# Optimization experiments

Measured on AMD Instinct MI355X. Metric: run time of the kernel, lower is better.

Reference implementation:

```python
import jax, jax.numpy as jnp
import numpy as np

B, C, W, H = 8, 256, 64, 64


def _conv1x1(x, w, b):
    # 1x1 conv == per-pixel channel GEMM. x: [B,C,W,H], w: [O,C], b: [O]
    return jnp.einsum('oc,bchw->bohw', w, x) + b[None, :, None, None]


def setup_inputs() -> dict:
    key = jax.random.key(0)
    ks = jax.random.split(key, 9)
    s = 1.0 / np.sqrt(C)
    return {
        'queries': jax.random.normal(ks[0], (B, C, W, H), dtype=jnp.float32),
        'keys': jax.random.normal(ks[1], (B, C, W, H), dtype=jnp.float32),
        'mask': jax.random.uniform(ks[2], (B, 1, W, H), dtype=jnp.float32),
        'Wq': jax.random.normal(ks[3], (C, C), dtype=jnp.float32) * s,
        'bq': jax.random.normal(ks[4], (C,), dtype=jnp.float32) * 0.01,
        'Wk': jax.random.normal(ks[5], (C, C), dtype=jnp.float32) * s,
        'bk': jax.random.normal(ks[6], (C,), dtype=jnp.float32) * 0.01,
        'Wv': jax.random.normal(ks[7], (C, C), dtype=jnp.float32) * s,
        'bv': jax.random.normal(ks[8], (C,), dtype=jnp.float32) * 0.01,
    }


def reference(queries, keys, mask, Wq, bq, Wk, bk, Wv, bv):
    b, c, w, h = queries.shape
    n = w * h
    q = _conv1x1(queries, Wq, bq).reshape(b, c, n)   # [B,C,N]
    k = _conv1x1(keys, Wk, bk).reshape(b, c, n)      # [B,C,N]
    v = _conv1x1(keys, Wv, bv).reshape(b, c, n)      # [B,C,N]
    # mask spatial size equals feature size -> interpolate(scale_factor=1) is identity
    m = mask.reshape(b, n)                            # [B,N]
    # scores[b,i,j] = <q_i, k_j>; torch's repeated mask multiplies row i by mask[i]
    scores = jnp.einsum('bcq,bck->bqk', q, k) * m[:, :, None]
    attn_w = jax.nn.softmax(scores, axis=-1)          # softmax over key dim
    attn = jnp.einsum('bqk,bck->bcq', attn_w, v).reshape(b, c, w, h)
    return queries * mask + (1.0 - mask) * attn
```

## Files before the change

kernel.cpp:

```cpp
#include <hip/hip_runtime.h>

typedef __attribute__((ext_vector_type(8))) _Float16 half8;
typedef __attribute__((ext_vector_type(4))) _Float16 half4;
typedef __attribute__((ext_vector_type(4))) float f32x4;

#define CDIM 256
#define NDIM 4096
#define MFMAH(a, b, c) __builtin_amdgcn_mfma_f32_16x16x32_f16((a), (b), (c), 0, 0, 0)

__global__ void cast_w_kernel(const float* __restrict__ Wq,
                              const float* __restrict__ Wk,
                              const float* __restrict__ Wv,
                              _Float16* __restrict__ Wc) {
  int t = blockIdx.x * 256 + threadIdx.x;
  int mat = t >> 14;
  int idx = (t & 16383) * 4;
  const float* W = (mat == 0) ? Wq : (mat == 1 ? Wk : Wv);
  float4 w = *(const float4*)(W + idx);
  half4 h = {(_Float16)w.x, (_Float16)w.y, (_Float16)w.z, (_Float16)w.w};
  *(half4*)(Wc + mat * 65536 + idx) = h;
}

__global__ __launch_bounds__(256, 2) void proj_kernel(
    const float* __restrict__ queries, const float* __restrict__ keys,
    const _Float16* __restrict__ Wc,
    const float* __restrict__ bq, const float* __restrict__ bk,
    const float* __restrict__ bv,
    _Float16* __restrict__ Qh, _Float16* __restrict__ Kh,
    _Float16* __restrict__ Vh)
{
  const int z = blockIdx.z, p = z >> 3, b = z & 7;
  const float* __restrict__ X = (p == 0) ? queries : keys;
  const _Float16* __restrict__ W = Wc + p * 65536;
  const float* __restrict__ bias = (p == 0) ? bq : (p == 1 ? bk : bv);
  const int n0 = blockIdx.x * 128;

  __shared__ __align__(16) _Float16 Xs[128][264];

  const int tid = threadIdx.x;
  const int wv = tid >> 6, lane = tid & 63, l16 = lane & 15, quad = lane >> 4;

#pragma unroll
  for (int it = 0; it < 32; ++it) {
    int id = tid + it * 256;
    int c = id >> 5, n4 = id & 31;
    float4 x = *(const float4*)&X[((size_t)(b * CDIM + c)) * NDIM + n0 + n4 * 4];
    Xs[n4 * 4 + 0][c] = (_Float16)x.x;
    Xs[n4 * 4 + 1][c] = (_Float16)x.y;
    Xs[n4 * 4 + 2][c] = (_Float16)x.z;
    Xs[n4 * 4 + 3][c] = (_Float16)x.w;
  }
  __syncthreads();

  f32x4 acc[4][8];
#pragma unroll
  for (int og = 0; og < 4; ++og)
#pragma unroll
    for (int ng = 0; ng < 8; ++ng) acc[og][ng] = (f32x4){0.f, 0.f, 0.f, 0.f};

#pragma unroll
  for (int kc = 0; kc < 8; ++kc) {
    half8 wf[4], xf[8];
#pragma unroll
    for (int og = 0; og < 4; ++og)
      wf[og] = *(const half8*)(W + (wv * 64 + og * 16 + l16) * CDIM + kc * 32 + quad * 8);
#pragma unroll
    for (int ng = 0; ng < 8; ++ng)
      xf[ng] = *(const half8*)&Xs[ng * 16 + l16][kc * 32 + quad * 8];
#pragma unroll
    for (int og = 0; og < 4; ++og)
#pragma unroll
      for (int ng = 0; ng < 8; ++ng)
        acc[og][ng] = MFMAH(wf[og], xf[ng], acc[og][ng]);
  }

#pragma unroll
  for (int og = 0; og < 4; ++og) {
    float4 b4 = *(const float4*)&bias[wv * 64 + og * 16 + quad * 4];
#pragma unroll
    for (int ng = 0; ng < 8; ++ng) {
      const int n = n0 + ng * 16 + l16;
      if (p == 2) {
#pragma unroll
        for (int r = 0; r < 4; ++r) {
          int o = wv * 64 + og * 16 + quad * 4 + r;
          float y = acc[og][ng][r] + ((const float*)&b4)[r];
          Vh[((size_t)(b * CDIM + o)) * NDIM + n] = (_Float16)y;
        }
      } else {
        half4 h4;
#pragma unroll
        for (int r = 0; r < 4; ++r)
          h4[r] = (_Float16)(acc[og][ng][r] + ((const float*)&b4)[r]);
        size_t idx = ((size_t)(b * NDIM + n)) * CDIM + wv * 64 + og * 16 + quad * 4;
        if (p == 0) *(half4*)&Qh[idx] = h4;
        else        *(half4*)&Kh[idx] = h4;
      }
    }
  }
}

__global__ __launch_bounds__(256, 2) void attn_kernel(
    const float* __restrict__ queries, const float* __restrict__ mask,
    const _Float16* __restrict__ Qh, const _Float16* __restrict__ Kh,
    const _Float16* __restrict__ Vh, float* __restrict__ out)
{
  const int blk = blockIdx.x, b = blk & 7, it = blk >> 3;
  const int i0 = it * 64;

  __shared__ __align__(16) _Float16 Ks[64][264];
  __shared__ __align__(16) _Float16 Vs[256][72];
  __shared__ __align__(16) _Float16 Ps[64][72];
  __shared__ __align__(16) float Al[64];
  __shared__ __align__(16) float Li[64];

  const int tid = threadIdx.x;
  const int wv = tid >> 6, lane = tid & 63, l16 = lane & 15, quad = lane >> 4;

  half8 qf[8];
  {
    const size_t qrow = ((size_t)(b * NDIM + i0 + wv * 16 + l16)) * CDIM;
#pragma unroll
    for (int kc = 0; kc < 8; ++kc)
      qf[kc] = *(const half8*)(Qh + qrow + kc * 32 + quad * 8);
  }
  const float mval = mask[(size_t)b * NDIM + i0 + wv * 16 + l16];
  float m_run = -1e30f, l_run = 0.f;

  f32x4 O[4][4];
#pragma unroll
  for (int g = 0; g < 4; ++g)
#pragma unroll
    for (int cg = 0; cg < 4; ++cg) O[g][cg] = (f32x4){0.f, 0.f, 0.f, 0.f};

  const _Float16* __restrict__ Kb = Kh + (size_t)b * NDIM * CDIM;
  const _Float16* __restrict__ Vbp = Vh + (size_t)b * CDIM * NDIM;

  for (int jt = 0; jt < 64; ++jt) {
    const int j0 = jt * 64;
    __syncthreads();
#pragma unroll
    for (int it2 = 0; it2 < 8; ++it2) {
      int id = tid + it2 * 256;
      int j = id >> 5, c8 = id & 31;
      *(uint4*)&Ks[j][c8 * 8] = *(const uint4*)(Kb + (size_t)(j0 + j) * CDIM + c8 * 8);
    }
#pragma unroll
    for (int it2 = 0; it2 < 8; ++it2) {
      int id = tid + it2 * 256;
      int c = id >> 3, j8 = id & 7;
      *(uint4*)&Vs[c][j8 * 8] = *(const uint4*)(Vbp + (size_t)c * NDIM + j0 + j8 * 8);
    }
    __syncthreads();

    f32x4 s[4];
#pragma unroll
    for (int js = 0; js < 4; ++js) s[js] = (f32x4){0.f, 0.f, 0.f, 0.f};
#pragma unroll
    for (int kc = 0; kc < 8; ++kc) {
#pragma unroll
      for (int js = 0; js < 4; ++js) {
        half8 kf = *(const half8*)&Ks[js * 16 + l16][kc * 32 + quad * 8];
        s[js] = MFMAH(kf, qf[kc], s[js]);
      }
    }

    float a[16];
    float mx = -1e30f;
#pragma unroll
    for (int js = 0; js < 4; ++js)
#pragma unroll
      for (int r = 0; r < 4; ++r) {
        float v = s[js][r] * mval;
        a[js * 4 + r] = v;
        mx = fmaxf(mx, v);
      }
    mx = fmaxf(mx, __shfl_xor(mx, 16));
    mx = fmaxf(mx, __shfl_xor(mx, 32));
    const float mnew = fmaxf(m_run, mx);
    const float alpha = __expf(m_run - mnew);
    m_run = mnew;
    float psum = 0.f;
#pragma unroll
    for (int js = 0; js < 4; ++js) {
      float p0 = __expf(a[js * 4 + 0] - mnew);
      float p1 = __expf(a[js * 4 + 1] - mnew);
      float p2 = __expf(a[js * 4 + 2] - mnew);
      float p3 = __expf(a[js * 4 + 3] - mnew);
      psum += (p0 + p1) + (p2 + p3);
      half4 hp = {(_Float16)p0, (_Float16)p1, (_Float16)p2, (_Float16)p3};
      *(half4*)&Ps[wv * 16 + l16][js * 16 + quad * 4] = hp;
    }
    psum += __shfl_xor(psum, 16);
    psum += __shfl_xor(psum, 32);
    l_run = l_run * alpha + psum;
    if (quad == 0) Al[wv * 16 + l16] = alpha;
    __syncthreads();

    f32x4 av[4];
#pragma unroll
    for (int g = 0; g < 4; ++g) av[g] = *(const f32x4*)&Al[g * 16 + quad * 4];
#pragma unroll
    for (int g = 0; g < 4; ++g)
#pragma unroll
      for (int cg = 0; cg < 4; ++cg)
#pragma unroll
        for (int r = 0; r < 4; ++r) O[g][cg][r] *= av[g][r];
#pragma unroll
    for (int kk = 0; kk < 2; ++kk) {
      half8 pa[4], vf[4];
#pragma unroll
      for (int g = 0; g < 4; ++g)
        pa[g] = *(const half8*)&Ps[g * 16 + l16][kk * 32 + quad * 8];
#pragma unroll
      for (int cg = 0; cg < 4; ++cg)
        vf[cg] = *(const half8*)&Vs[wv * 64 + cg * 16 + l16][kk * 32 + quad * 8];
#pragma unroll
      for (int g = 0; g < 4; ++g)
#pragma unroll
        for (int cg = 0; cg < 4; ++cg)
          O[g][cg] = MFMAH(pa[g], vf[cg], O[g][cg]);
    }
  }

  if (quad == 0) Li[wv * 16 + l16] = 1.0f / l_run;
  __syncthreads();
#pragma unroll
  for (int g = 0; g < 4; ++g) {
    f32x4 li4 = *(const f32x4*)&Li[g * 16 + quad * 4];
    const int i = i0 + g * 16 + quad * 4;
    float4 m4 = *(const float4*)&mask[(size_t)b * NDIM + i];
#pragma unroll
    for (int cg = 0; cg < 4; ++cg) {
      const int c = wv * 64 + cg * 16 + l16;
      const size_t base = ((size_t)(b * CDIM + c)) * NDIM + i;
      float4 q4 = *(const float4*)(queries + base);
      float4 o4;
      o4.x = q4.x * m4.x + (1.f - m4.x) * (O[g][cg][0] * li4[0]);
      o4.y = q4.y * m4.y + (1.f - m4.y) * (O[g][cg][1] * li4[1]);
      o4.z = q4.z * m4.z + (1.f - m4.z) * (O[g][cg][2] * li4[2]);
      o4.w = q4.w * m4.w + (1.f - m4.w) * (O[g][cg][3] * li4[3]);
      *(float4*)(out + base) = o4;
    }
  }
}

extern "C" void kernel_launch(void* const* d_in, const int* in_sizes, int n_in,
                              void* d_out, int out_size, void* d_ws, size_t ws_size,
                              hipStream_t stream) {
  const float* queries = (const float*)d_in[0];
  const float* keys    = (const float*)d_in[1];
  const float* mask    = (const float*)d_in[2];
  const float* Wq = (const float*)d_in[3];
  const float* bq = (const float*)d_in[4];
  const float* Wk = (const float*)d_in[5];
  const float* bk = (const float*)d_in[6];
  const float* Wv = (const float*)d_in[7];
  const float* bv = (const float*)d_in[8];
  float* out = (float*)d_out;

  const size_t elems = (size_t)8 * NDIM * CDIM;
  _Float16* Qh = (_Float16*)d_ws;
  _Float16* Kh = Qh + elems;
  _Float16* Vh = Kh + elems;
  _Float16* Wc = Vh + elems;

  cast_w_kernel<<<dim3(192), 256, 0, stream>>>(Wq, Wk, Wv, Wc);
  proj_kernel<<<dim3(32, 1, 24), 256, 0, stream>>>(
      queries, keys, Wc, bq, bk, bv, Qh, Kh, Vh);
  attn_kernel<<<dim3(512), 256, 0, stream>>>(
      queries, mask, Qh, Kh, Vh, out);
}
```

Measured before the change: 358.6 us.

## Use 32x32 MFMA for QK scores with split-key warps and restructure X loads

The QK^T score computation now uses 32x32x16 MFMA tiles. Each wave covers 32 query rows by 32 keys, so the key tile is split between wave pairs, and row max and sum are combined through shared memory at the cost of an extra barrier per tile. Separately, the projection kernel's X staging now reads one pixel column across 8 channels per thread and writes packed half8 values to LDS, replacing scattered scalar half stores. This trades fewer LDS operations per MFMA for more query registers (16 half8 fragments) and an additional synchronisation in the softmax step.

```diff
diff --git a/kernel.cpp b/kernel.cpp
--- a/kernel.cpp
+++ b/kernel.cpp
@@ -3,10 +3,12 @@
 typedef __attribute__((ext_vector_type(8))) _Float16 half8;
 typedef __attribute__((ext_vector_type(4))) _Float16 half4;
 typedef __attribute__((ext_vector_type(4))) float f32x4;
+typedef __attribute__((ext_vector_type(16))) float f32x16;
 
 #define CDIM 256
 #define NDIM 4096
 #define MFMAH(a, b, c) __builtin_amdgcn_mfma_f32_16x16x32_f16((a), (b), (c), 0, 0, 0)
+#define MFMA32(a, b, c) __builtin_amdgcn_mfma_f32_32x32x16_f16((a), (b), (c), 0, 0, 0)
 
 __global__ void cast_w_kernel(const float* __restrict__ Wq,
                               const float* __restrict__ Wk,
@@ -40,15 +42,17 @@
   const int tid = threadIdx.x;
   const int wv = tid >> 6, lane = tid & 63, l16 = lane & 15, quad = lane >> 4;
 
-#pragma unroll
-  for (int it = 0; it < 32; ++it) {
-    int id = tid + it * 256;
-    int c = id >> 5, n4 = id & 31;
-    float4 x = *(const float4*)&X[((size_t)(b * CDIM + c)) * NDIM + n0 + n4 * 4];
-    Xs[n4 * 4 + 0][c] = (_Float16)x.x;
-    Xs[n4 * 4 + 1][c] = (_Float16)x.y;
-    Xs[n4 * 4 + 2][c] = (_Float16)x.z;
-    Xs[n4 * 4 + 3][c] = (_Float16)x.w;
+  {
+    const int nn = tid & 127, ch = tid >> 7;
+#pragma unroll
+    for (int it2 = 0; it2 < 16; ++it2) {
+      const int c0 = it2 * 16 + ch * 8;
+      const float* src = X + ((size_t)(b * CDIM + c0)) * NDIM + n0 + nn;
+      half8 hx;
+#pragma unroll
+      for (int k = 0; k < 8; ++k) hx[k] = (_Float16)src[(size_t)k * NDIM];
+      *(half8*)&Xs[nn][c0] = hx;
+    }
   }
   __syncthreads();
 
@@ -113,18 +117,23 @@
   __shared__ __align__(16) _Float16 Ps[64][72];
   __shared__ __align__(16) float Al[64];
   __shared__ __align__(16) float Li[64];
+  __shared__ __align__(16) float Mp[2][64];
+  __shared__ __align__(16) float Sp[2][64];
 
   const int tid = threadIdx.x;
   const int wv = tid >> 6, lane = tid & 63, l16 = lane & 15, quad = lane >> 4;
-
-  half8 qf[8];
+  const int l32 = lane & 31, h = lane >> 5;
+  const int jq = wv & 1, iq = wv >> 1;
+  const int myi = iq * 32 + l32;
+
+  half8 qf[16];
   {
-    const size_t qrow = ((size_t)(b * NDIM + i0 + wv * 16 + l16)) * CDIM;
-#pragma unroll
-    for (int kc = 0; kc < 8; ++kc)
-      qf[kc] = *(const half8*)(Qh + qrow + kc * 32 + quad * 8);
-  }
-  const float mval = mask[(size_t)b * NDIM + i0 + wv * 16 + l16];
+    const size_t qrow = ((size_t)(b * NDIM + i0 + myi)) * CDIM;
+#pragma unroll
+    for (int kk = 0; kk < 16; ++kk)
+      qf[kk] = *(const half8*)(Qh + qrow + kk * 16 + h * 8);
+  }
+  const float mval = mask[(size_t)b * NDIM + i0 + myi];
   float m_run = -1e30f, l_run = 0.f;
 
   f32x4 O[4][4];
@@ -153,49 +162,42 @@
     }
     __syncthreads();
 
-    f32x4 s[4];
-#pragma unroll
-    for (int js = 0; js < 4; ++js) s[js] = (f32x4){0.f, 0.f, 0.f, 0.f};
-#pragma unroll
-    for (int kc = 0; kc < 8; ++kc) {
-#pragma unroll
-      for (int js = 0; js < 4; ++js) {
-        half8 kf = *(const half8*)&Ks[js * 16 + l16][kc * 32 + quad * 8];
-        s[js] = MFMAH(kf, qf[kc], s[js]);
-      }
-    }
-
-    float a[16];
+    f32x16 st = {};
+#pragma unroll
+    for (int kk = 0; kk < 16; ++kk) {
+      half8 kf = *(const half8*)&Ks[jq * 32 + l32][kk * 16 + h * 8];
+      st = MFMA32(kf, qf[kk], st);
+    }
+
     float mx = -1e30f;
 #pragma unroll
-    for (int js = 0; js < 4; ++js)
-#pragma unroll
-      for (int r = 0; r < 4; ++r) {
-        float v = s[js][r] * mval;
-        a[js * 4 + r] = v;
-        mx = fmaxf(mx, v);
-      }
-    mx = fmaxf(mx, __shfl_xor(mx, 16));
+    for (int r = 0; r < 16; ++r) mx = fmaxf(mx, st[r] * mval);
     mx = fmaxf(mx, __shfl_xor(mx, 32));
-    const float mnew = fmaxf(m_run, mx);
+    if (h == 0) Mp[jq][myi] = mx;
+    __syncthreads();
+
+    const float mxall = fmaxf(Mp[0][myi], Mp[1][myi]);
+    const float mnew = fmaxf(m_run, mxall);
     const float alpha = __expf(m_run - mnew);
     m_run = mnew;
+    if (jq == 0 && h == 0) Al[myi] = alpha;
+
     float psum = 0.f;
 #pragma unroll
-    for (int js = 0; js < 4; ++js) {
-      float p0 = __expf(a[js * 4 + 0] - mnew);
-      float p1 = __expf(a[js * 4 + 1] - mnew);
-      float p2 = __expf(a[js * 4 + 2] - mnew);
-      float p3 = __expf(a[js * 4 + 3] - mnew);
+    for (int g2 = 0; g2 < 4; ++g2) {
+      float p0 = __expf(st[g2 * 4 + 0] * mval - mnew);
+      float p1 = __expf(st[g2 * 4 + 1] * mval - mnew);
+      float p2 = __expf(st[g2 * 4 + 2] * mval - mnew);
+      float p3 = __expf(st[g2 * 4 + 3] * mval - mnew);
       psum += (p0 + p1) + (p2 + p3);
       half4 hp = {(_Float16)p0, (_Float16)p1, (_Float16)p2, (_Float16)p3};
-      *(half4*)&Ps[wv * 16 + l16][js * 16 + quad * 4] = hp;
-    }
-    psum += __shfl_xor(psum, 16);
+      *(half4*)&Ps[myi][jq * 32 + g2 * 8 + h * 4] = hp;
+    }
     psum += __shfl_xor(psum, 32);
-    l_run = l_run * alpha + psum;
-    if (quad == 0) Al[wv * 16 + l16] = alpha;
-    __syncthreads();
+    if (h == 0) Sp[jq][myi] = psum;
+    __syncthreads();
+
+    l_run = l_run * alpha + Sp[0][myi] + Sp[1][myi];
 
     f32x4 av[4];
 #pragma unroll
@@ -223,7 +225,7 @@
     }
   }
 
-  if (quad == 0) Li[wv * 16 + l16] = 1.0f / l_run;
+  if (jq == 0 && h == 0) Li[myi] = 1.0f / l_run;
   __syncthreads();
 #pragma unroll
   for (int g = 0; g < 4; ++g) {
```

Measured after the change: 535.8 us. +49.4%, slower.

## Load V fragments straight to registers and double-buffer P to drop a barrier

Applied to the files above, without the earlier changes.

Each wave now loads its own 64-channel slice of V from global memory directly into MFMA register fragments, instead of staging the whole V tile through shared memory. The P and alpha shared buffers are double-buffered by iteration parity, which removes the barrier at the top of the key-tile loop. This cuts LDS traffic and one block-wide sync per tile. In exchange, the V global loads are less coalesced (64-byte row segments), and 32 extra VGPRs stay live across the score MFMAs, which may cause spills under the two-blocks-per-CU launch bound.

```diff
diff --git a/kernel.cpp b/kernel.cpp
--- a/kernel.cpp
+++ b/kernel.cpp
@@ -109,9 +109,8 @@
   const int i0 = it * 64;
 
   __shared__ __align__(16) _Float16 Ks[64][264];
-  __shared__ __align__(16) _Float16 Vs[256][72];
-  __shared__ __align__(16) _Float16 Ps[64][72];
-  __shared__ __align__(16) float Al[64];
+  __shared__ __align__(16) _Float16 Ps[2][64][72];
+  __shared__ __align__(16) float Al[2][64];
   __shared__ __align__(16) float Li[64];
 
   const int tid = threadIdx.x;
@@ -134,23 +133,23 @@
     for (int cg = 0; cg < 4; ++cg) O[g][cg] = (f32x4){0.f, 0.f, 0.f, 0.f};
 
   const _Float16* __restrict__ Kb = Kh + (size_t)b * NDIM * CDIM;
-  const _Float16* __restrict__ Vbp = Vh + (size_t)b * CDIM * NDIM;
+  const _Float16* __restrict__ Vw = Vh + ((size_t)(b * CDIM + wv * 64)) * NDIM;
 
   for (int jt = 0; jt < 64; ++jt) {
     const int j0 = jt * 64;
-    __syncthreads();
+    const int pb = jt & 1;
 #pragma unroll
     for (int it2 = 0; it2 < 8; ++it2) {
       int id = tid + it2 * 256;
       int j = id >> 5, c8 = id & 31;
       *(uint4*)&Ks[j][c8 * 8] = *(const uint4*)(Kb + (size_t)(j0 + j) * CDIM + c8 * 8);
     }
-#pragma unroll
-    for (int it2 = 0; it2 < 8; ++it2) {
-      int id = tid + it2 * 256;
-      int c = id >> 3, j8 = id & 7;
-      *(uint4*)&Vs[c][j8 * 8] = *(const uint4*)(Vbp + (size_t)c * NDIM + j0 + j8 * 8);
-    }
+    half8 vf[2][4];
+#pragma unroll
+    for (int kk = 0; kk < 2; ++kk)
+#pragma unroll
+      for (int cg = 0; cg < 4; ++cg)
+        vf[kk][cg] = *(const half8*)(Vw + (size_t)(cg * 16 + l16) * NDIM + j0 + kk * 32 + quad * 8);
     __syncthreads();
 
     f32x4 s[4];
@@ -189,17 +188,17 @@
       float p3 = __expf(a[js * 4 + 3] - mnew);
       psum += (p0 + p1) + (p2 + p3);
       half4 hp = {(_Float16)p0, (_Float16)p1, (_Float16)p2, (_Float16)p3};
-      *(half4*)&Ps[wv * 16 + l16][js * 16 + quad * 4] = hp;
+      *(half4*)&Ps[pb][wv * 16 + l16][js * 16 + quad * 4] = hp;
     }
     psum += __shfl_xor(psum, 16);
     psum += __shfl_xor(psum, 32);
     l_run = l_run * alpha + psum;
-    if (quad == 0) Al[wv * 16 + l16] = alpha;
+    if (quad == 0) Al[pb][wv * 16 + l16] = alpha;
     __syncthreads();
 
     f32x4 av[4];
 #pragma unroll
-    for (int g = 0; g < 4; ++g) av[g] = *(const f32x4*)&Al[g * 16 + quad * 4];
+    for (int g = 0; g < 4; ++g) av[g] = *(const f32x4*)&Al[pb][g * 16 + quad * 4];
 #pragma unroll
     for (int g = 0; g < 4; ++g)
 #pragma unroll
@@ -208,18 +207,15 @@
         for (int r = 0; r < 4; ++r) O[g][cg][r] *= av[g][r];
 #pragma unroll
     for (int kk = 0; kk < 2; ++kk) {
-      half8 pa[4], vf[4];
+      half8 pa[4];
 #pragma unroll
       for (int g = 0; g < 4; ++g)
-        pa[g] = *(const half8*)&Ps[g * 16 + l16][kk * 32 + quad * 8];
-#pragma unroll
-      for (int cg = 0; cg < 4; ++cg)
-        vf[cg] = *(const half8*)&Vs[wv * 64 + cg * 16 + l16][kk * 32 + quad * 8];
+        pa[g] = *(const half8*)&Ps[pb][g * 16 + l16][kk * 32 + quad * 8];
 #pragma unroll
       for (int g = 0; g < 4; ++g)
 #pragma unroll
         for (int cg = 0; cg < 4; ++cg)
-          O[g][cg] = MFMAH(pa[g], vf[cg], O[g][cg]);
+          O[g][cg] = MFMAH(pa[g], vf[kk][cg], O[g][cg]);
     }
   }
 
```

Measured after the change: 331.7 us. 7.5% less time.
